# Kernel optimization log

Measured on AMD Instinct MI355X. Metric: run time of the kernel, lower is better.

## Reference

```python
import jax, jax.numpy as jnp
import numpy as np

N, K_IN, K_OUT = 200000, 8, 4
E, D, H, O = 800000, 64, 128, 1


def setup_inputs() -> dict:
    key = jax.random.key(0)
    ks = jax.random.split(key, 8)
    edges = jax.random.normal(ks[0], (E, D), dtype=jnp.float32)
    in_idx = jax.random.randint(ks[1], (N, K_IN), 0, E, dtype=jnp.int32)
    in_mask = jax.random.randint(ks[2], (N, K_IN), 0, 2, dtype=jnp.int32)
    out_idx = jax.random.randint(ks[3], (N, K_OUT), 0, E, dtype=jnp.int32)
    out_mask = jax.random.randint(ks[4], (N, K_OUT), 0, 2, dtype=jnp.int32)
    # FC stack params: layer0 takes 2*D (edge feat ++ pooled attention context)
    W0 = jax.random.normal(ks[5], (H, 2 * D), dtype=jnp.float32) * (1.0 / np.sqrt(2 * D))
    b0 = jnp.zeros((H,), dtype=jnp.float32)
    W1 = jax.random.normal(ks[6], (H, H), dtype=jnp.float32) * (1.0 / np.sqrt(H))
    b1 = jnp.zeros((H,), dtype=jnp.float32)
    Wout = jax.random.normal(ks[7], (O, H), dtype=jnp.float32) * (1.0 / np.sqrt(H))
    bout = jnp.zeros((O,), dtype=jnp.float32)
    return {"edges": edges, "in_idx": in_idx, "in_mask": in_mask,
            "out_idx": out_idx, "out_mask": out_mask,
            "W0": W0, "b0": b0, "W1": W1, "b1": b1, "Wout": Wout, "bout": bout}


def _forward(edges, in_idx, in_mask, out_idx, out_mask, W0, b0, W1, b1, Wout, bout):
    d = edges.shape[1]
    mbool = in_mask.astype(bool)                       # [N, K_in]
    mf = in_mask.astype(edges.dtype)[..., None]        # [N, K_in, 1]
    # gather per-node in-edge sets: [N, K_in, D]
    Ein = edges[in_idx]
    # self-attention over the in-edge set (query=key=value=in_edges)
    scores = jnp.einsum('nqd,nkd->nqk', Ein, Ein) / jnp.sqrt(jnp.asarray(d, edges.dtype))
    scores = jnp.where(mbool[:, None, :], scores, jnp.asarray(-1e9, edges.dtype))
    attn = jax.nn.softmax(scores, axis=-1)
    att_out = jnp.einsum('nqk,nkd->nqd', attn, Ein)    # [N, K_in, D]
    # pool attended rows over valid queries -> weighted_in_edges [N, D]
    denom = jnp.maximum(mf.sum(axis=1), 1.0)
    pooled = (att_out * mf).sum(axis=1) / denom
    # per out-edge: concat(edge_feat, pooled) -> MLP
    Eout = edges[out_idx]                              # [N, K_out, D]
    pooled_b = jnp.broadcast_to(pooled[:, None, :], Eout.shape)
    x = jnp.concatenate([Eout, pooled_b], axis=-1)     # [N, K_out, 2D]
    h = jax.nn.relu(jnp.einsum('nkd,hd->nkh', x, W0) + b0)
    h = jax.nn.relu(jnp.einsum('nkh,gh->nkg', h, W1) + b1)
    y = jnp.einsum('nkh,oh->nko', h, Wout) + bout      # [N, K_out, O]
    y = y * out_mask.astype(y.dtype)[..., None]        # zero padded out-edges
    return y.reshape(-1, y.shape[-1])                  # [N*K_out, O]


def reference(edges, in_idx, in_mask, out_idx, out_mask, W0, b0, W1, b1, Wout, bout):
    return _forward(edges, in_idx, in_mask, out_idx, out_mask, W0, b0, W1, b1, Wout, bout)
```

## Files before the change

kernel.cpp:

```cpp
#include <hip/hip_runtime.h>
#include <math.h>

#define D 64
#define H 128
#define KIN 8
#define KOUT 4
#define NPB 16
#define ROWS (NPB*KOUT)
#define THREADS 256
#define WAVES 4
#define NPW (NPB/WAVES)
#define XLDB 136
#define ELD 68

typedef __attribute__((ext_vector_type(8))) short short8v;
typedef __attribute__((ext_vector_type(4))) float f32x4;

__device__ inline unsigned short f2bf(float f) {
    union { float f; unsigned u; } v; v.f = f;
    unsigned r = v.u + 0x7FFF + ((v.u >> 16) & 1);
    return (unsigned short)(r >> 16);
}
__device__ inline float bf2f(unsigned short h) {
    union { unsigned u; float f; } v; v.u = ((unsigned)h) << 16; return v.f;
}

__global__ void convert_w_kernel(const float* __restrict__ W0,
                                 const float* __restrict__ W1,
                                 unsigned short* __restrict__ Wbf) {
    const int i = blockIdx.x * 256 + threadIdx.x;
    const float v = (i < H*H) ? W0[i] : W1[i - H*H];
    Wbf[i] = f2bf(v);
}

__global__ __launch_bounds__(THREADS, 4) void encoder_kernel(
    const float* __restrict__ edges,
    const int*   __restrict__ in_idx,
    const int*   __restrict__ in_mask,
    const int*   __restrict__ out_idx,
    const int*   __restrict__ out_mask,
    const float* __restrict__ b0, const float* __restrict__ b1,
    const float* __restrict__ Wout, const float* __restrict__ bout,
    const unsigned short* __restrict__ Wbf,
    float* __restrict__ out, int N)
{
    __shared__ unsigned short xbuf[ROWS][XLDB];
    __shared__ float eins[WAVES][KIN][ELD];
    __shared__ float omaskf[ROWS];

    const int tid  = threadIdx.x;
    const int wave = tid >> 6;
    const int lane = tid & 63;
    const int nodeBase = blockIdx.x * NPB;

    const int q   = lane >> 3;
    const int kk8 = lane & 7;
    for (int it = 0; it < NPW; ++it) {
        const int nl = wave * NPW + it;
        const int n  = nodeBase + nl;
        if (n < N) {
            #pragma unroll
            for (int e = 0; e < KIN; ++e) {
                const int idx = in_idx[n*KIN + e];
                eins[wave][e][lane] = edges[(size_t)idx * D + lane];
            }
            float denom = 0.f;
            #pragma unroll
            for (int e = 0; e < KIN; ++e) denom += (float)in_mask[n*KIN + e];
            denom = fmaxf(denom, 1.f);
            const float mk_k = (float)in_mask[n*KIN + kk8];
            const float mk_q = (float)in_mask[n*KIN + q];

            float s = 0.f;
            #pragma unroll
            for (int d4 = 0; d4 < D; d4 += 4) {
                const float4 a = *(const float4*)&eins[wave][q][d4];
                const float4 b = *(const float4*)&eins[wave][kk8][d4];
                s += a.x*b.x + a.y*b.y + a.z*b.z + a.w*b.w;
            }
            s *= 0.125f;
            if (mk_k == 0.f) s = -1e9f;

            float mx = s;
            #pragma unroll
            for (int off = 1; off < 8; off <<= 1) mx = fmaxf(mx, __shfl_xor(mx, off));
            const float ex = __expf(s - mx);
            float sum = ex;
            #pragma unroll
            for (int off = 1; off < 8; off <<= 1) sum += __shfl_xor(sum, off);

            float wk = mk_q * (ex / sum);
            #pragma unroll
            for (int off = 8; off < 64; off <<= 1) wk += __shfl_xor(wk, off);

            float p = 0.f;
            #pragma unroll
            for (int j = 0; j < KIN; ++j) p += __shfl(wk, j) * eins[wave][j][lane];
            p /= denom;
            const unsigned short pb = f2bf(p);

            #pragma unroll
            for (int j = 0; j < KOUT; ++j) {
                const int oi = out_idx[n*KOUT + j];
                xbuf[nl*KOUT + j][lane]     = f2bf(edges[(size_t)oi * D + lane]);
                xbuf[nl*KOUT + j][D + lane] = pb;
            }
            if (lane < KOUT) omaskf[nl*KOUT + lane] = (float)out_mask[n*KOUT + lane];
        }
    }
    __syncthreads();

    const int rowbase = (wave >> 1) * 32;
    const int colbase = (wave & 1) * 64;
    const int l15  = lane & 15;
    const int kofs = (lane >> 4) * 8;
    const int rrow = (lane >> 4) * 4;

    #pragma unroll
    for (int layer = 0; layer < 2; ++layer) {
        const unsigned short* __restrict__ Wl = Wbf + layer * (H*H);
        const float* __restrict__ bl = layer ? b1 : b0;

        f32x4 acc[2][4];
        #pragma unroll
        for (int ct = 0; ct < 4; ++ct) {
            const float bv = bl[colbase + ct*16 + l15];
            #pragma unroll
            for (int r = 0; r < 2; ++r) acc[r][ct] = (f32x4){bv, bv, bv, bv};
        }

        #pragma unroll
        for (int ks = 0; ks < 4; ++ks) {
            short8v bf[4];
            #pragma unroll
            for (int ct = 0; ct < 4; ++ct)
                bf[ct] = *(const short8v*)&Wl[(size_t)(colbase + ct*16 + l15) * H + ks*32 + kofs];
            #pragma unroll
            for (int r = 0; r < 2; ++r) {
                const short8v a = *(const short8v*)&xbuf[rowbase + r*16 + l15][ks*32 + kofs];
                #pragma unroll
                for (int ct = 0; ct < 4; ++ct)
                    acc[r][ct] = __builtin_amdgcn_mfma_f32_16x16x32_bf16(a, bf[ct], acc[r][ct], 0, 0, 0);
            }
        }
        __syncthreads();
        #pragma unroll
        for (int r = 0; r < 2; ++r)
            #pragma unroll
            for (int ct = 0; ct < 4; ++ct)
                #pragma unroll
                for (int j = 0; j < 4; ++j)
                    xbuf[rowbase + r*16 + rrow + j][colbase + ct*16 + l15] =
                        f2bf(fmaxf(acc[r][ct][j], 0.f));
        __syncthreads();
    }

    {
        const int row = tid >> 2;
        const int kq  = tid & 3;
        float p = 0.f;
        #pragma unroll
        for (int m = 0; m < 4; ++m) {
            const int k0 = kq*32 + m*8;
            const short8v hv = *(const short8v*)&xbuf[row][k0];
            const float4 w0 = *(const float4*)&Wout[k0];
            const float4 w1 = *(const float4*)&Wout[k0 + 4];
            p += bf2f((unsigned short)hv[0]) * w0.x + bf2f((unsigned short)hv[1]) * w0.y
               + bf2f((unsigned short)hv[2]) * w0.z + bf2f((unsigned short)hv[3]) * w0.w
               + bf2f((unsigned short)hv[4]) * w1.x + bf2f((unsigned short)hv[5]) * w1.y
               + bf2f((unsigned short)hv[6]) * w1.z + bf2f((unsigned short)hv[7]) * w1.w;
        }
        p += __shfl_xor(p, 1);
        p += __shfl_xor(p, 2);
        if (kq == 0) {
            const long long grow = (long long)nodeBase * KOUT + row;
            if (grow < (long long)N * KOUT)
                out[grow] = (p + bout[0]) * omaskf[row];
        }
    }
}

extern "C" void kernel_launch(void* const* d_in, const int* in_sizes, int n_in,
                              void* d_out, int out_size, void* d_ws, size_t ws_size,
                              hipStream_t stream)
{
    const float* edges  = (const float*)d_in[0];
    const int* in_idx   = (const int*)d_in[1];
    const int* in_mask  = (const int*)d_in[2];
    const int* out_idx  = (const int*)d_in[3];
    const int* out_mask = (const int*)d_in[4];
    const float* W0   = (const float*)d_in[5];
    const float* b0   = (const float*)d_in[6];
    const float* W1   = (const float*)d_in[7];
    const float* b1   = (const float*)d_in[8];
    const float* Wout = (const float*)d_in[9];
    const float* bout = (const float*)d_in[10];
    float* out = (float*)d_out;
    unsigned short* Wbf = (unsigned short*)d_ws;

    const int nNodes = in_sizes[1] / KIN;
    convert_w_kernel<<<(2*H*H + 255) / 256, 256, 0, stream>>>(W0, W1, Wbf);
    const int grid = (nNodes + NPB - 1) / NPB;
    encoder_kernel<<<grid, THREADS, 0, stream>>>(
        edges, in_idx, in_mask, out_idx, out_mask,
        b0, b1, Wout, bout, Wbf, out, nNodes);
}
```

Before: 573.1 us.

## Compute in-edge attention scores with bf16 MFMA, two nodes per wave

The attention phase now handles two nodes at a time per wave. Their 16 in-edge rows are staged as bf16 and the 16x16 Gram matrix is computed with two MFMA instructions, masking the cross-node blocks, in place of the per-lane scalar dot products. Gather indices are loaded once per lane and broadcast with shuffles, which exposes more independent gathers in flight. This cuts the VALU and LDS work of the attention step, but scores now use bf16 inputs, the node bounds check is gone (N must be a multiple of 16), and the register count rises.

```diff
diff --git a/kernel.cpp b/kernel.cpp
--- a/kernel.cpp
+++ b/kernel.cpp
@@ -11,7 +11,7 @@
 #define WAVES 4
 #define NPW (NPB/WAVES)
 #define XLDB 136
-#define ELD 68
+#define ELD16 72
 
 typedef __attribute__((ext_vector_type(8))) short short8v;
 typedef __attribute__((ext_vector_type(4))) float f32x4;
@@ -20,9 +20,6 @@
     union { float f; unsigned u; } v; v.f = f;
     unsigned r = v.u + 0x7FFF + ((v.u >> 16) & 1);
     return (unsigned short)(r >> 16);
-}
-__device__ inline float bf2f(unsigned short h) {
-    union { unsigned u; float f; } v; v.u = ((unsigned)h) << 16; return v.f;
 }
 
 __global__ void convert_w_kernel(const float* __restrict__ W0,
@@ -44,8 +41,8 @@
     const unsigned short* __restrict__ Wbf,
     float* __restrict__ out, int N)
 {
-    __shared__ unsigned short xbuf[ROWS][XLDB];
-    __shared__ float eins[WAVES][KIN][ELD];
+    __shared__ __align__(16) unsigned short xbuf[ROWS][XLDB];
+    __shared__ __align__(16) unsigned short eins[WAVES][16][ELD16];
     __shared__ float omaskf[ROWS];
 
     const int tid  = threadIdx.x;
@@ -53,59 +50,85 @@
     const int lane = tid & 63;
     const int nodeBase = blockIdx.x * NPB;
 
-    const int q   = lane >> 3;
-    const int kk8 = lane & 7;
-    for (int it = 0; it < NPW; ++it) {
-        const int nl = wave * NPW + it;
-        const int n  = nodeBase + nl;
-        if (n < N) {
-            #pragma unroll
-            for (int e = 0; e < KIN; ++e) {
-                const int idx = in_idx[n*KIN + e];
-                eins[wave][e][lane] = edges[(size_t)idx * D + lane];
-            }
-            float denom = 0.f;
-            #pragma unroll
-            for (int e = 0; e < KIN; ++e) denom += (float)in_mask[n*KIN + e];
-            denom = fmaxf(denom, 1.f);
-            const float mk_k = (float)in_mask[n*KIN + kk8];
-            const float mk_q = (float)in_mask[n*KIN + q];
-
-            float s = 0.f;
-            #pragma unroll
-            for (int d4 = 0; d4 < D; d4 += 4) {
-                const float4 a = *(const float4*)&eins[wave][q][d4];
-                const float4 b = *(const float4*)&eins[wave][kk8][d4];
-                s += a.x*b.x + a.y*b.y + a.z*b.z + a.w*b.w;
-            }
-            s *= 0.125f;
-            if (mk_k == 0.f) s = -1e9f;
-
-            float mx = s;
-            #pragma unroll
-            for (int off = 1; off < 8; off <<= 1) mx = fmaxf(mx, __shfl_xor(mx, off));
-            const float ex = __expf(s - mx);
-            float sum = ex;
-            #pragma unroll
-            for (int off = 1; off < 8; off <<= 1) sum += __shfl_xor(sum, off);
-
-            float wk = mk_q * (ex / sum);
-            #pragma unroll
-            for (int off = 8; off < 64; off <<= 1) wk += __shfl_xor(wk, off);
-
-            float p = 0.f;
-            #pragma unroll
-            for (int j = 0; j < KIN; ++j) p += __shfl(wk, j) * eins[wave][j][lane];
-            p /= denom;
-            const unsigned short pb = f2bf(p);
-
-            #pragma unroll
-            for (int j = 0; j < KOUT; ++j) {
-                const int oi = out_idx[n*KOUT + j];
-                xbuf[nl*KOUT + j][lane]     = f2bf(edges[(size_t)oi * D + lane]);
-                xbuf[nl*KOUT + j][D + lane] = pb;
-            }
-            if (lane < KOUT) omaskf[nl*KOUT + lane] = (float)out_mask[n*KOUT + lane];
+    const int col = lane & 15;
+    const int grp = lane >> 4;
+
+    for (int it = 0; it < 2; ++it) {
+        const int nl0 = wave * NPW + it * 2;
+        const int n0  = nodeBase + nl0;
+
+        const int   idx_l  = in_idx [n0*KIN  + col];
+        const float mkcol  = (float)in_mask[n0*KIN  + col];
+        const int   oidx_l = out_idx[n0*KOUT + (lane & 7)];
+
+        float ein_r[16];
+        #pragma unroll
+        for (int r = 0; r < 16; ++r) {
+            const int gi = __shfl(idx_l, r);
+            ein_r[r] = edges[(size_t)gi * D + lane];
+            eins[wave][r][lane] = f2bf(ein_r[r]);
+        }
+        #pragma unroll
+        for (int r = 0; r < 8; ++r) {
+            const int gi = __shfl(oidx_l, r);
+            xbuf[nl0*KOUT + r][lane] = f2bf(edges[(size_t)gi * D + lane]);
+        }
+        if (lane < 2*KOUT) omaskf[nl0*KOUT + lane] = (float)out_mask[n0*KOUT + lane];
+
+        const short8v f0 = *(const short8v*)&eins[wave][col][grp*8];
+        const short8v f1 = *(const short8v*)&eins[wave][col][32 + grp*8];
+        f32x4 sc = (f32x4){0.f, 0.f, 0.f, 0.f};
+        sc = __builtin_amdgcn_mfma_f32_16x16x32_bf16(f0, f0, sc, 0, 0, 0);
+        sc = __builtin_amdgcn_mfma_f32_16x16x32_bf16(f1, f1, sc, 0, 0, 0);
+
+        float s0, s1, s2, s3;
+        {
+            const bool kv = (mkcol > 0.f);
+            #define MSK(jj, sv) { const int row = grp*4 + jj; \
+                const bool ok = kv && ((row < 8) == (col < 8)); \
+                sv = ok ? sc[jj] * 0.125f : -1e9f; }
+            MSK(0, s0) MSK(1, s1) MSK(2, s2) MSK(3, s3)
+            #undef MSK
+        }
+        float m0=s0, m1=s1, m2=s2, m3=s3;
+        #pragma unroll
+        for (int off = 1; off < 16; off <<= 1) {
+            m0 = fmaxf(m0, __shfl_xor(m0, off));
+            m1 = fmaxf(m1, __shfl_xor(m1, off));
+            m2 = fmaxf(m2, __shfl_xor(m2, off));
+            m3 = fmaxf(m3, __shfl_xor(m3, off));
+        }
+        float e0=__expf(s0-m0), e1=__expf(s1-m1), e2=__expf(s2-m2), e3=__expf(s3-m3);
+        float t0=e0, t1=e1, t2=e2, t3=e3;
+        #pragma unroll
+        for (int off = 1; off < 16; off <<= 1) {
+            t0 += __shfl_xor(t0, off); t1 += __shfl_xor(t1, off);
+            t2 += __shfl_xor(t2, off); t3 += __shfl_xor(t3, off);
+        }
+        float wsum = __shfl(mkcol, grp*4 + 0) * (e0 / t0)
+                   + __shfl(mkcol, grp*4 + 1) * (e1 / t1)
+                   + __shfl(mkcol, grp*4 + 2) * (e2 / t2)
+                   + __shfl(mkcol, grp*4 + 3) * (e3 / t3);
+        wsum += __shfl_xor(wsum, 16);
+        wsum += __shfl_xor(wsum, 32);
+
+        float dn = mkcol;
+        dn += __shfl_xor(dn, 1); dn += __shfl_xor(dn, 2); dn += __shfl_xor(dn, 4);
+        const float dnA = fmaxf(__shfl(dn, 0), 1.f);
+        const float dnB = fmaxf(__shfl(dn, 8), 1.f);
+
+        float pA = 0.f, pB = 0.f;
+        #pragma unroll
+        for (int k = 0; k < 8; ++k) {
+            pA += __shfl(wsum, k)     * ein_r[k];
+            pB += __shfl(wsum, 8 + k) * ein_r[8 + k];
+        }
+        const unsigned short pbA = f2bf(pA / dnA);
+        const unsigned short pbB = f2bf(pB / dnB);
+        #pragma unroll
+        for (int j = 0; j < KOUT; ++j) {
+            xbuf[ nl0   *KOUT + j][D + lane] = pbA;
+            xbuf[(nl0+1)*KOUT + j][D + lane] = pbB;
         }
     }
     __syncthreads();
@@ -165,10 +188,17 @@
             const short8v hv = *(const short8v*)&xbuf[row][k0];
             const float4 w0 = *(const float4*)&Wout[k0];
             const float4 w1 = *(const float4*)&Wout[k0 + 4];
-            p += bf2f((unsigned short)hv[0]) * w0.x + bf2f((unsigned short)hv[1]) * w0.y
-               + bf2f((unsigned short)hv[2]) * w0.z + bf2f((unsigned short)hv[3]) * w0.w
-               + bf2f((unsigned short)hv[4]) * w1.x + bf2f((unsigned short)hv[5]) * w1.y
-               + bf2f((unsigned short)hv[6]) * w1.z + bf2f((unsigned short)hv[7]) * w1.w;
+            union { unsigned u; float f; } c;
+            float acc8 = 0.f;
+            c.u = ((unsigned)(unsigned short)hv[0]) << 16; acc8 += c.f * w0.x;
+            c.u = ((unsigned)(unsigned short)hv[1]) << 16; acc8 += c.f * w0.y;
+            c.u = ((unsigned)(unsigned short)hv[2]) << 16; acc8 += c.f * w0.z;
+            c.u = ((unsigned)(unsigned short)hv[3]) << 16; acc8 += c.f * w0.w;
+            c.u = ((unsigned)(unsigned short)hv[4]) << 16; acc8 += c.f * w1.x;
+            c.u = ((unsigned)(unsigned short)hv[5]) << 16; acc8 += c.f * w1.y;
+            c.u = ((unsigned)(unsigned short)hv[6]) << 16; acc8 += c.f * w1.z;
+            c.u = ((unsigned)(unsigned short)hv[7]) << 16; acc8 += c.f * w1.w;
+            p += acc8;
         }
         p += __shfl_xor(p, 1);
         p += __shfl_xor(p, 2);
```

After: 643.7 us. 1.12x slower.
